# Kernel optimization log

Hardware: AMD Instinct MI355X
Metric: run time of the kernel (lower is better)

Reference implementation:

```python
import jax, jax.numpy as jnp
import numpy as np
import math

B, S, D = 2, 2048, 1024
H = 16
HD = D // H  # 64


def setup_inputs() -> dict:
    key = jax.random.key(0)
    ks = jax.random.split(key, 5)
    scale = 0.02
    x = jax.random.normal(ks[0], (B, S, D), dtype=jnp.float32)
    # torch Linear weights stored as [in, out] (already transposed)
    w_qkv = jax.random.normal(ks[1], (D, 3 * D), dtype=jnp.float32) * scale
    b_qkv = jnp.zeros((3 * D,), dtype=jnp.float32)
    w_proj = jax.random.normal(ks[2], (D, D), dtype=jnp.float32) * scale
    b_proj = jnp.zeros((D,), dtype=jnp.float32)
    return {"x": x, "w_qkv": w_qkv, "b_qkv": b_qkv, "w_proj": w_proj, "b_proj": b_proj}


def reference(x, w_qkv, b_qkv, w_proj, b_proj):
    b, s, d = x.shape
    qkv = x @ w_qkv + b_qkv                              # [B,S,3D]
    qkv = qkv.reshape(b, s, 3, H, HD)
    qkv = jnp.transpose(qkv, (2, 0, 3, 1, 4))            # [3,B,H,S,HD]
    q, k, v = qkv[0], qkv[1], qkv[2]
    present = jnp.concatenate([k, v], axis=0)            # [2B,H,S,HD]
    # scaled causal attention, full [B,H,S,S] scores as in the original
    attn = jnp.einsum('bhqd,bhkd->bhqk', q, k) * (1.0 / math.sqrt(HD))
    causal = jnp.tril(jnp.ones((s, s), dtype=bool))
    attn = jnp.where(causal[None, None], attn, -jnp.inf)
    attn = jax.nn.softmax(attn, axis=-1)
    out = jnp.einsum('bhqk,bhkd->bhqd', attn, v)         # [B,H,S,HD]
    out = jnp.transpose(out, (0, 2, 1, 3)).reshape(b, s, d)
    out = out @ w_proj + b_proj                          # NOTE: original module has project layer; see notes
    return (out, present)
```

## Files before the change

kernel.cpp:

```cpp
#include <hip/hip_runtime.h>
#include <hip/hip_bf16.h>

typedef short s16x8 __attribute__((ext_vector_type(8)));
typedef short s16x4 __attribute__((ext_vector_type(4)));
typedef float f32x4 __attribute__((ext_vector_type(4)));
typedef float f32x16 __attribute__((ext_vector_type(16)));
typedef unsigned int u32x4 __attribute__((ext_vector_type(4)));

#define S_LEN 2048
#define DMODEL 1024
#define NHEAD 16
#define HDIM 64
#define OUT_ELEMS 4194304
#define HEAD_ELEMS 4194304
#define SCALE_LOG2 0.1803368801111204f

__device__ inline short f2bf(float f) {
  __hip_bfloat16 h = __float2bfloat16(f);
  return __builtin_bit_cast(short, h);
}

__device__ inline f32x4 mfma16(s16x8 a, s16x8 b, f32x4 c) {
  return __builtin_amdgcn_mfma_f32_16x16x32_bf16(a, b, c, 0, 0, 0);
}
__device__ inline f32x16 mfma32(s16x8 a, s16x8 b, f32x16 c) {
  return __builtin_amdgcn_mfma_f32_32x32x16_bf16(a, b, c, 0, 0, 0);
}

__global__ __launch_bounds__(256) void transpose_cvt(
    const float* __restrict__ in, short* __restrict__ out, int R, int C) {
  int g = blockIdx.x * 256 + threadIdx.x;
  int c = g % C;
  int r0 = (g / C) * 8;
  s16x8 v;
#pragma unroll
  for (int j = 0; j < 8; j++) v[j] = f2bf(in[(size_t)(r0 + j) * C + c]);
  *(s16x8*)&out[(size_t)c * R + r0] = v;
}

template <int MODE, bool AF32>
__global__ __launch_bounds__(256) void gemm_bt(
    const void* __restrict__ Araw, const short* __restrict__ Bt,
    const float* __restrict__ bias, short* __restrict__ Ob0,
    float* __restrict__ Of, short* __restrict__ VtOut,
    short* __restrict__ KwOut, int M, int N, int K) {
  __shared__ short As[128][40];
  __shared__ short Bs[128][40];
  const int t = threadIdx.x;
  const int lane = t & 63;
  const int wid = t >> 6;
  const int wr = wid >> 1, wc = wid & 1;
  const int l16 = lane & 15, lg = lane >> 4;
  const int mbase = blockIdx.y * 128;
  const int nbase = blockIdx.x * 128;

  f32x4 acc[4][4];
#pragma unroll
  for (int m = 0; m < 4; m++)
#pragma unroll
    for (int n = 0; n < 4; n++) acc[m][n] = (f32x4){0.f, 0.f, 0.f, 0.f};

  const int srow = t >> 2;
  const int skc = (t & 3) * 8;

  for (int k0 = 0; k0 < K; k0 += 32) {
    s16x8 a0, a1;
    if constexpr (AF32) {
      const float* Af = (const float*)Araw;
      const float* p0 = &Af[(size_t)(mbase + srow) * K + k0 + skc];
      const float* p1 = &Af[(size_t)(mbase + srow + 64) * K + k0 + skc];
      f32x4 x00 = *(const f32x4*)p0, x01 = *(const f32x4*)(p0 + 4);
      f32x4 x10 = *(const f32x4*)p1, x11 = *(const f32x4*)(p1 + 4);
#pragma unroll
      for (int j = 0; j < 4; j++) {
        a0[j] = f2bf(x00[j]); a0[4 + j] = f2bf(x01[j]);
        a1[j] = f2bf(x10[j]); a1[4 + j] = f2bf(x11[j]);
      }
    } else {
      const short* Ab = (const short*)Araw;
      a0 = *(const s16x8*)&Ab[(size_t)(mbase + srow) * K + k0 + skc];
      a1 = *(const s16x8*)&Ab[(size_t)(mbase + srow + 64) * K + k0 + skc];
    }
    s16x8 b0 = *(const s16x8*)&Bt[(size_t)(nbase + srow) * K + k0 + skc];
    s16x8 b1 = *(const s16x8*)&Bt[(size_t)(nbase + srow + 64) * K + k0 + skc];
    __syncthreads();
    *(s16x8*)&As[srow][skc] = a0;
    *(s16x8*)&As[srow + 64][skc] = a1;
    *(s16x8*)&Bs[srow][skc] = b0;
    *(s16x8*)&Bs[srow + 64][skc] = b1;
    __syncthreads();
    s16x8 af[4], bfr[4];
#pragma unroll
    for (int m = 0; m < 4; m++)
      af[m] = *(const s16x8*)&As[wr * 64 + m * 16 + l16][lg * 8];
#pragma unroll
    for (int n = 0; n < 4; n++)
      bfr[n] = *(const s16x8*)&Bs[wc * 64 + n * 16 + l16][lg * 8];
#pragma unroll
    for (int m = 0; m < 4; m++)
#pragma unroll
      for (int n = 0; n < 4; n++)
        acc[m][n] = mfma16(af[m], bfr[n], acc[m][n]);
  }

#pragma unroll
  for (int m = 0; m < 4; m++) {
#pragma unroll
    for (int n = 0; n < 4; n++) {
      int gcol = nbase + wc * 64 + n * 16 + l16;
      float bv = bias[gcol];
      int part = gcol >> 10;
      int cin = gcol & 1023;
      int h = cin >> 6, hd = cin & 63;
      int grow0 = mbase + wr * 64 + m * 16 + lg * 4;
      float vr[4];
#pragma unroll
      for (int r = 0; r < 4; r++) vr[r] = acc[m][n][r] + bv;
      if (MODE == 0) {
        int bb = grow0 >> 11, s0 = grow0 & 2047;
        size_t base = ((size_t)(bb * NHEAD + h) * S_LEN + s0) * HDIM + hd;
        if (part == 0) {
#pragma unroll
          for (int r = 0; r < 4; r++)
            Ob0[base + (size_t)r * HDIM] = f2bf(vr[r] * SCALE_LOG2);
        } else if (part == 1) {
#pragma unroll
          for (int r = 0; r < 4; r++) Of[base + (size_t)r * HDIM] = vr[r];
          if (KwOut) {
#pragma unroll
            for (int r = 0; r < 4; r++)
              KwOut[base + (size_t)r * HDIM] = f2bf(vr[r]);
          }
        } else {
#pragma unroll
          for (int r = 0; r < 4; r++)
            Of[HEAD_ELEMS + base + (size_t)r * HDIM] = vr[r];
          s16x4 pk;
#pragma unroll
          for (int r = 0; r < 4; r++) pk[r] = f2bf(vr[r]);
          int w32 = s0 & 31;
          int nw = ((w32 >> 4) << 4) | ((w32 & 4) << 1) | ((w32 & 8) >> 1);
          int sperm = (s0 & ~31) | nw;
          *(s16x4*)&VtOut[((size_t)(bb * NHEAD + h) * HDIM + hd) * S_LEN +
                          sperm] = pk;
        }
      } else {
#pragma unroll
        for (int r = 0; r < 4; r++) Of[(size_t)(grow0 + r) * N + gcol] = vr[r];
      }
    }
  }
}

__global__ __launch_bounds__(256, 2) void attn_fwd_kbf16(
    const short* __restrict__ Q, const short* __restrict__ K,
    const short* __restrict__ Vt, short* __restrict__ AO) {
  __shared__ short Ks[2][64][64];
  __shared__ short Vs[2][64][64];

  const int p = blockIdx.x;
  const int bh = p & 31;
  const int seg = (p >> 5) & 7;
  const int qi = (p < 256) ? (15 - seg) : seg;
  const int qb = qi * 128;
  const int nt = 2 * qi + 2;

  const int tid = threadIdx.x;
  const int w = tid >> 6;
  const int lane = tid & 63;
  const int l32 = lane & 31;
  const int hi = lane >> 5;
  const int rsub = lane >> 3;
  const int sub = lane & 7;

  const short* Qb = Q + (size_t)bh * (S_LEN * HDIM);
  const short* Kb = K + (size_t)bh * (S_LEN * HDIM);
  const short* Vb = Vt + (size_t)bh * (HDIM * S_LEN);
  const int b = bh >> 4, h = bh & 15;

  const int qrow = qb + 32 * w + l32;
  const int qminw = qb + 32 * w;
  const int qmaxw = qminw + 31;

  s16x8 qf[4];
#pragma unroll
  for (int c = 0; c < 4; c++)
    qf[c] = *(const s16x8*)&Qb[(size_t)qrow * HDIM + c * 16 + hi * 8];

  f32x16 acc0 = {0.f}, acc1 = {0.f};
  float m = -1e30f, ll = 0.f;

  s16x8 kreg[2], vreg[2];
  auto LOADT = [&](int kt) {
    const int kb = kt * 64;
#pragma unroll
    for (int c = 0; c < 2; c++) {
      int row = 16 * w + 8 * c + rsub;
      int gs = sub ^ (row & 7);
      kreg[c] = *(const s16x8*)&Kb[(size_t)(kb + row) * HDIM + gs * 8];
      vreg[c] = *(const s16x8*)&Vb[(size_t)row * S_LEN + kb + gs * 8];
    }
  };
  auto WRITET = [&](int bb) {
#pragma unroll
    for (int c = 0; c < 2; c++) {
      int row = 16 * w + 8 * c + rsub;
      *(s16x8*)&Ks[bb][row][sub * 8] = kreg[c];
      *(s16x8*)&Vs[bb][row][sub * 8] = vreg[c];
    }
  };

  LOADT(0);
  WRITET(0);
  __syncthreads();
  int cur = 0;

#pragma unroll 1
  for (int kt = 0; kt < nt; kt++) {
    const int kb = kt * 64;
    if (kt + 1 < nt) LOADT(kt + 1);
    if (kb <= qmaxw) {
      f32x16 S0 = {0.f}, S1 = {0.f};
#pragma unroll
      for (int c = 0; c < 4; c++) {
        int cs = c * 2 + hi;
        int r0 = l32;
        int r1 = 32 + l32;
        s16x8 k0 = *(const s16x8*)&Ks[cur][r0][(cs ^ (r0 & 7)) * 8];
        s16x8 k1 = *(const s16x8*)&Ks[cur][r1][(cs ^ (r1 & 7)) * 8];
        S0 = mfma32(k0, qf[c], S0);
        S1 = mfma32(k1, qf[c], S1);
      }
      if (kb + 63 > qminw) {
#pragma unroll
        for (int r = 0; r < 16; r++) {
          int key0 = kb + (r & 3) + 8 * (r >> 2) + 4 * hi;
          S0[r] = (key0 <= qrow) ? S0[r] : -1e30f;
          S1[r] = (key0 + 32 <= qrow) ? S1[r] : -1e30f;
        }
      }
      float t8[8];
#pragma unroll
      for (int r = 0; r < 8; r++)
        t8[r] = fmaxf(fmaxf(S0[2 * r], S0[2 * r + 1]),
                      fmaxf(S1[2 * r], S1[2 * r + 1]));
      float tmax = fmaxf(fmaxf(fmaxf(t8[0], t8[1]), fmaxf(t8[2], t8[3])),
                         fmaxf(fmaxf(t8[4], t8[5]), fmaxf(t8[6], t8[7])));
      tmax = fmaxf(tmax, __shfl_xor(tmax, 32));
      if (!__all(tmax <= m + 11.0f)) {
        float mn = fmaxf(m, tmax);
        float alpha = __builtin_amdgcn_exp2f(m - mn);
        ll *= alpha;
#pragma unroll
        for (int r = 0; r < 16; r++) {
          acc0[r] *= alpha;
          acc1[r] *= alpha;
        }
        m = mn;
      }
#pragma unroll
      for (int r = 0; r < 16; r++) {
        S0[r] = __builtin_amdgcn_exp2f(S0[r] - m);
        S1[r] = __builtin_amdgcn_exp2f(S1[r] - m);
      }
      float s8[8];
#pragma unroll
      for (int r = 0; r < 8; r++)
        s8[r] = (S0[2 * r] + S0[2 * r + 1]) + (S1[2 * r] + S1[2 * r + 1]);
      float rs = ((s8[0] + s8[1]) + (s8[2] + s8[3])) +
                 ((s8[4] + s8[5]) + (s8[6] + s8[7]));
      rs += __shfl_xor(rs, 32);
      ll += rs;
#pragma unroll
      for (int half = 0; half < 2; half++) {
        const f32x16& S = half ? S1 : S0;
        u32x4 pbAv, pbBv;
#pragma unroll
        for (int g = 0; g < 4; g++) {
          unsigned int lo = (unsigned short)f2bf(S[2 * g]);
          unsigned int h16 = (unsigned short)f2bf(S[2 * g + 1]);
          pbAv[g] = lo | (h16 << 16);
          unsigned int lo2 = (unsigned short)f2bf(S[8 + 2 * g]);
          unsigned int h162 = (unsigned short)f2bf(S[9 + 2 * g]);
          pbBv[g] = lo2 | (h162 << 16);
        }
#pragma unroll
        for (int gg = 0; gg < 2; gg++) {
          s16x8 pb = __builtin_bit_cast(s16x8, gg ? pbBv : pbAv);
          int cs = (half * 2 + gg) * 2 + hi;
          int v0r = l32;
          int v1r = 32 + l32;
          s16x8 va0 = *(const s16x8*)&Vs[cur][v0r][(cs ^ (v0r & 7)) * 8];
          s16x8 va1 = *(const s16x8*)&Vs[cur][v1r][(cs ^ (v1r & 7)) * 8];
          acc0 = mfma32(va0, pb, acc0);
          acc1 = mfma32(va1, pb, acc1);
        }
      }
    }
    if (kt + 1 < nt) WRITET(cur ^ 1);
    __syncthreads();
    cur ^= 1;
  }

  float inv = 1.f / ll;
  size_t rowbase = ((size_t)(b * S_LEN + qrow)) * DMODEL + h * HDIM;
#pragma unroll
  for (int g = 0; g < 4; g++) {
    s16x4 o0, o1;
#pragma unroll
    for (int u = 0; u < 4; u++) {
      o0[u] = f2bf(acc0[4 * g + u] * inv);
      o1[u] = f2bf(acc1[4 * g + u] * inv);
    }
    *(s16x4*)&AO[rowbase + 8 * g + 4 * hi] = o0;
    *(s16x4*)&AO[rowbase + 32 + 8 * g + 4 * hi] = o1;
  }
}

__global__ __launch_bounds__(256, 4) void attn_fwd_kf32(
    const short* __restrict__ Q, const float* __restrict__ Kraw,
    const short* __restrict__ Vt, short* __restrict__ AO) {
  __shared__ float XFER[2][64][37];
  const int p = blockIdx.x;
  const int xcd = p & 7;
  const int rank = p >> 3;
  const int bh = (xcd << 2) | (rank >> 5);
  const int pr = rank & 31;
  const int tid = threadIdx.x;
  const int w = tid >> 6;
  const int lane = tid & 63;
  const int l32 = lane & 31;
  const int hi = lane >> 5;
  const short* Qb = Q + (size_t)bh * (S_LEN * HDIM);
  const short* Vb = Vt + (size_t)bh * (HDIM * S_LEN);
  const float* Kb32 = Kraw + (size_t)bh * (S_LEN * HDIM);
  const int b = bh >> 4, h = bh & 15;

#pragma unroll 1
  for (int ph = 0; ph < 2; ph++) {
    const int j = ph ? pr : 63 - pr;
    const int qb = j * 32;
    s16x8 qf[4];
#pragma unroll
    for (int c = 0; c < 4; c++)
      qf[c] = *(const s16x8*)&Qb[(size_t)(qb + l32) * HDIM + c * 16 + hi * 8];
    f32x16 acc0 = {0.f}, acc1 = {0.f};
    float m = -1e30f, ll = 0.f;
#pragma unroll 1
    for (int kt = w; kt <= j; kt += 4) {
      const int kb = kt * 32;
      f32x16 S = {0.f};
#pragma unroll
      for (int c = 0; c < 4; c++) {
        const float* kr = &Kb32[(size_t)(kb + l32) * HDIM + c * 16 + hi * 8];
        f32x4 k0 = *(const f32x4*)kr, k1 = *(const f32x4*)(kr + 4);
        s16x8 kf;
#pragma unroll
        for (int u = 0; u < 4; u++) {
          kf[u] = f2bf(k0[u]);
          kf[4 + u] = f2bf(k1[u]);
        }
        S = mfma32(kf, qf[c], S);
      }
      const short* vr0 = &Vb[(size_t)l32 * S_LEN + kb + hi * 8];
      const short* vr1 = &Vb[(size_t)(32 + l32) * S_LEN + kb + hi * 8];
      s16x8 va00 = *(const s16x8*)vr0;
      s16x8 va01 = *(const s16x8*)(vr0 + 16);
      s16x8 va10 = *(const s16x8*)vr1;
      s16x8 va11 = *(const s16x8*)(vr1 + 16);
      if (kt == j) {
#pragma unroll
        for (int r = 0; r < 16; r++) {
          int keyl = (r & 3) + 8 * (r >> 2) + 4 * hi;
          S[r] = (keyl <= l32) ? S[r] : -1e30f;
        }
      }
      float t8[8];
#pragma unroll
      for (int r = 0; r < 8; r++) t8[r] = fmaxf(S[2 * r], S[2 * r + 1]);
      float tmax = fmaxf(fmaxf(fmaxf(t8[0], t8[1]), fmaxf(t8[2], t8[3])),
                         fmaxf(fmaxf(t8[4], t8[5]), fmaxf(t8[6], t8[7])));
      tmax = fmaxf(tmax, __shfl_xor(tmax, 32));
      if (!__all(tmax <= m + 11.0f)) {
        float mn = fmaxf(m, tmax);
        float alpha = __builtin_amdgcn_exp2f(m - mn);
        ll *= alpha;
#pragma unroll
        for (int r = 0; r < 16; r++) {
          acc0[r] *= alpha;
          acc1[r] *= alpha;
        }
        m = mn;
      }
#pragma unroll
      for (int r = 0; r < 16; r++) S[r] = __builtin_amdgcn_exp2f(S[r] - m);
      float s8[8];
#pragma unroll
      for (int r = 0; r < 8; r++) s8[r] = S[2 * r] + S[2 * r + 1];
      float rs = ((s8[0] + s8[1]) + (s8[2] + s8[3])) +
                 ((s8[4] + s8[5]) + (s8[6] + s8[7]));
      rs += __shfl_xor(rs, 32);
      ll += rs;
      u32x4 pb0v, pb1v;
#pragma unroll
      for (int g = 0; g < 4; g++) {
        unsigned int lo = (unsigned short)f2bf(S[2 * g]);
        unsigned int h16 = (unsigned short)f2bf(S[2 * g + 1]);
        pb0v[g] = lo | (h16 << 16);
        unsigned int lo2 = (unsigned short)f2bf(S[8 + 2 * g]);
        unsigned int h162 = (unsigned short)f2bf(S[9 + 2 * g]);
        pb1v[g] = lo2 | (h162 << 16);
      }
      s16x8 pb0 = __builtin_bit_cast(s16x8, pb0v);
      s16x8 pb1 = __builtin_bit_cast(s16x8, pb1v);
      acc0 = mfma32(va00, pb0, acc0);
      acc1 = mfma32(va10, pb0, acc1);
      acc0 = mfma32(va01, pb1, acc0);
      acc1 = mfma32(va11, pb1, acc1);
    }
    if (w & 1) {
      float* dst = &XFER[w >> 1][lane][0];
      dst[0] = m; dst[1] = ll;
#pragma unroll
      for (int r = 0; r < 16; r++) { dst[2 + r] = acc0[r]; dst[18 + r] = acc1[r]; }
    }
    __syncthreads();
    if (!(w & 1)) {
      const float* src = &XFER[w >> 1][lane][0];
      float m2 = src[0], l2 = src[1];
      float M = fmaxf(m, m2);
      float a1 = __builtin_amdgcn_exp2f(m - M);
      float a2 = __builtin_amdgcn_exp2f(m2 - M);
      ll = ll * a1 + l2 * a2;
#pragma unroll
      for (int r = 0; r < 16; r++) {
        acc0[r] = acc0[r] * a1 + src[2 + r] * a2;
        acc1[r] = acc1[r] * a1 + src[18 + r] * a2;
      }
      m = M;
    }
    __syncthreads();
    if (w == 2) {
      float* dst = &XFER[0][lane][0];
      dst[0] = m; dst[1] = ll;
#pragma unroll
      for (int r = 0; r < 16; r++) { dst[2 + r] = acc0[r]; dst[18 + r] = acc1[r]; }
    }
    __syncthreads();
    if (w == 0) {
      const float* src = &XFER[0][lane][0];
      float m2 = src[0], l2 = src[1];
      float M = fmaxf(m, m2);
      float a1 = __builtin_amdgcn_exp2f(m - M);
      float a2 = __builtin_amdgcn_exp2f(m2 - M);
      ll = ll * a1 + l2 * a2;
#pragma unroll
      for (int r = 0; r < 16; r++) {
        acc0[r] = acc0[r] * a1 + src[2 + r] * a2;
        acc1[r] = acc1[r] * a1 + src[18 + r] * a2;
      }
      float inv = 1.f / ll;
      size_t rowbase = ((size_t)(b * S_LEN + qb + l32)) * DMODEL + h * HDIM;
#pragma unroll
      for (int g = 0; g < 4; g++) {
        s16x4 o0, o1;
#pragma unroll
        for (int u = 0; u < 4; u++) {
          o0[u] = f2bf(acc0[4 * g + u] * inv);
          o1[u] = f2bf(acc1[4 * g + u] * inv);
        }
        *(s16x4*)&AO[rowbase + 8 * g + 4 * hi] = o0;
        *(s16x4*)&AO[rowbase + 32 + 8 * g + 4 * hi] = o1;
      }
    }
    __syncthreads();
  }
}

extern "C" void kernel_launch(void* const* d_in, const int* in_sizes, int n_in,
                              void* d_out, int out_size, void* d_ws,
                              size_t ws_size, hipStream_t stream) {
  const float* x = (const float*)d_in[0];
  const float* w_qkv = (const float*)d_in[1];
  const float* b_qkv = (const float*)d_in[2];
  const float* w_proj = (const float*)d_in[3];
  const float* b_proj = (const float*)d_in[4];
  float* out = (float*)d_out;
  float* presentK = out + OUT_ELEMS;

  short* ws = (short*)d_ws;
  const bool kbf16 = ws_size >= (size_t)35651584;

  short *Qw, *Vt, *wprojT, *wqkvT, *attnout, *Kw;
  if (kbf16) {
    Qw = ws;
    Kw = ws + 4194304;
    Vt = ws + 8388608;
    wprojT = ws + 12582912;
    wqkvT = ws + 13631488;
    attnout = ws + 13631488;
  } else {
    if (ws_size < (size_t)27262976) return;
    Qw = ws;
    Vt = ws + 4194304;
    wprojT = ws + 8388608;
    wqkvT = ws + 9437184;
    attnout = ws + 9437184;
    Kw = nullptr;
  }

  transpose_cvt<<<dim3(1536), 256, 0, stream>>>(w_qkv, wqkvT, 1024, 3072);
  transpose_cvt<<<dim3(512), 256, 0, stream>>>(w_proj, wprojT, 1024, 1024);
  gemm_bt<0, true><<<dim3(24, 32), 256, 0, stream>>>(
      x, wqkvT, b_qkv, Qw, presentK, Vt, Kw, 4096, 3072, 1024);
  if (kbf16)
    attn_fwd_kbf16<<<dim3(512), 256, 0, stream>>>(Qw, Kw, Vt, attnout);
  else
    attn_fwd_kf32<<<dim3(1024), 256, 0, stream>>>(Qw, presentK, Vt, attnout);
  gemm_bt<1, false><<<dim3(8, 32), 256, 0, stream>>>(
      attnout, wprojT, b_proj, nullptr, out, nullptr, nullptr, 4096, 1024,
      1024);
}
```

Before: 131.0 us.

## Pre-convert x to bf16 and stage GEMM tiles via direct global-to-LDS loads

Adds a separate kernel that converts x to bf16 into the output buffer as scratch, so the QKV GEMM reads only bf16 operands. Both GEMMs now use the global_load_lds builtin to copy 16-byte chunks straight into shared memory, bypassing registers. The padding is removed from the LDS tiles, which raises the risk of bank conflicts on fragment reads. It also adds an extra launch and an extra pass over x.

```diff
diff --git a/kernel.cpp b/kernel.cpp
--- a/kernel.cpp
+++ b/kernel.cpp
@@ -27,6 +27,27 @@
   return __builtin_amdgcn_mfma_f32_32x32x16_bf16(a, b, c, 0, 0, 0);
 }
 
+typedef __attribute__((address_space(1))) const void gvoid;
+typedef __attribute__((address_space(3))) void lvoid;
+__device__ inline void gload_lds16(const void* g, void* l) {
+  __builtin_amdgcn_global_load_lds((gvoid*)g, (lvoid*)l, 16, 0, 0);
+}
+
+__global__ __launch_bounds__(256) void cvt_bf16(const float* __restrict__ in,
+                                                short* __restrict__ out) {
+  int g = blockIdx.x * 256 + threadIdx.x;
+  const float* p = &in[(size_t)g * 8];
+  f32x4 a = *(const f32x4*)p;
+  f32x4 b = *(const f32x4*)(p + 4);
+  s16x8 v;
+#pragma unroll
+  for (int j = 0; j < 4; j++) {
+    v[j] = f2bf(a[j]);
+    v[4 + j] = f2bf(b[j]);
+  }
+  *(s16x8*)&out[(size_t)g * 8] = v;
+}
+
 __global__ __launch_bounds__(256) void transpose_cvt(
     const float* __restrict__ in, short* __restrict__ out, int R, int C) {
   int g = blockIdx.x * 256 + threadIdx.x;
@@ -38,14 +59,14 @@
   *(s16x8*)&out[(size_t)c * R + r0] = v;
 }
 
-template <int MODE, bool AF32>
+template <int MODE>
 __global__ __launch_bounds__(256) void gemm_bt(
-    const void* __restrict__ Araw, const short* __restrict__ Bt,
+    const short* __restrict__ A, const short* __restrict__ Bt,
     const float* __restrict__ bias, short* __restrict__ Ob0,
     float* __restrict__ Of, short* __restrict__ VtOut,
     short* __restrict__ KwOut, int M, int N, int K) {
-  __shared__ short As[128][40];
-  __shared__ short Bs[128][40];
+  __shared__ short As[128 * 32];
+  __shared__ short Bs[128 * 32];
   const int t = threadIdx.x;
   const int lane = t & 63;
   const int wid = t >> 6;
@@ -60,42 +81,29 @@
 #pragma unroll
     for (int n = 0; n < 4; n++) acc[m][n] = (f32x4){0.f, 0.f, 0.f, 0.f};
 
-  const int srow = t >> 2;
-  const int skc = (t & 3) * 8;
+  const int srow = lane >> 2;
+  const int scol = (lane & 3) * 8;
+  const short* Ag = &A[(size_t)(mbase + wid * 32 + srow) * K + scol];
+  const short* Bg = &Bt[(size_t)(nbase + wid * 32 + srow) * K + scol];
+  short* AsW0 = &As[(wid * 32) * 32];
+  short* AsW1 = &As[(wid * 32 + 16) * 32];
+  short* BsW0 = &Bs[(wid * 32) * 32];
+  short* BsW1 = &Bs[(wid * 32 + 16) * 32];
 
   for (int k0 = 0; k0 < K; k0 += 32) {
-    s16x8 a0, a1;
-    if constexpr (AF32) {
-      const float* Af = (const float*)Araw;
-      const float* p0 = &Af[(size_t)(mbase + srow) * K + k0 + skc];
-      const float* p1 = &Af[(size_t)(mbase + srow + 64) * K + k0 + skc];
-      f32x4 x00 = *(const f32x4*)p0, x01 = *(const f32x4*)(p0 + 4);
-      f32x4 x10 = *(const f32x4*)p1, x11 = *(const f32x4*)(p1 + 4);
-#pragma unroll
-      for (int j = 0; j < 4; j++) {
-        a0[j] = f2bf(x00[j]); a0[4 + j] = f2bf(x01[j]);
-        a1[j] = f2bf(x10[j]); a1[4 + j] = f2bf(x11[j]);
-      }
-    } else {
-      const short* Ab = (const short*)Araw;
-      a0 = *(const s16x8*)&Ab[(size_t)(mbase + srow) * K + k0 + skc];
-      a1 = *(const s16x8*)&Ab[(size_t)(mbase + srow + 64) * K + k0 + skc];
-    }
-    s16x8 b0 = *(const s16x8*)&Bt[(size_t)(nbase + srow) * K + k0 + skc];
-    s16x8 b1 = *(const s16x8*)&Bt[(size_t)(nbase + srow + 64) * K + k0 + skc];
-    __syncthreads();
-    *(s16x8*)&As[srow][skc] = a0;
-    *(s16x8*)&As[srow + 64][skc] = a1;
-    *(s16x8*)&Bs[srow][skc] = b0;
-    *(s16x8*)&Bs[srow + 64][skc] = b1;
+    __syncthreads();
+    gload_lds16(Ag + k0, AsW0);
+    gload_lds16(Ag + (size_t)16 * K + k0, AsW1);
+    gload_lds16(Bg + k0, BsW0);
+    gload_lds16(Bg + (size_t)16 * K + k0, BsW1);
     __syncthreads();
     s16x8 af[4], bfr[4];
 #pragma unroll
     for (int m = 0; m < 4; m++)
-      af[m] = *(const s16x8*)&As[wr * 64 + m * 16 + l16][lg * 8];
+      af[m] = *(const s16x8*)&As[(wr * 64 + m * 16 + l16) * 32 + lg * 8];
 #pragma unroll
     for (int n = 0; n < 4; n++)
-      bfr[n] = *(const s16x8*)&Bs[wc * 64 + n * 16 + l16][lg * 8];
+      bfr[n] = *(const s16x8*)&Bs[(wc * 64 + n * 16 + l16) * 32 + lg * 8];
 #pragma unroll
     for (int m = 0; m < 4; m++)
 #pragma unroll
@@ -488,6 +496,8 @@
   float* out = (float*)d_out;
   float* presentK = out + OUT_ELEMS;
 
+  short* xbf = (short*)out;
+
   short* ws = (short*)d_ws;
   const bool kbf16 = ws_size >= (size_t)35651584;
 
@@ -509,15 +519,16 @@
     Kw = nullptr;
   }
 
+  cvt_bf16<<<dim3(2048), 256, 0, stream>>>(x, xbf);
   transpose_cvt<<<dim3(1536), 256, 0, stream>>>(w_qkv, wqkvT, 1024, 3072);
   transpose_cvt<<<dim3(512), 256, 0, stream>>>(w_proj, wprojT, 1024, 1024);
-  gemm_bt<0, true><<<dim3(24, 32), 256, 0, stream>>>(
-      x, wqkvT, b_qkv, Qw, presentK, Vt, Kw, 4096, 3072, 1024);
+  gemm_bt<0><<<dim3(24, 32), 256, 0, stream>>>(
+      xbf, wqkvT, b_qkv, Qw, presentK, Vt, Kw, 4096, 3072, 1024);
   if (kbf16)
     attn_fwd_kbf16<<<dim3(512), 256, 0, stream>>>(Qw, Kw, Vt, attnout);
   else
     attn_fwd_kf32<<<dim3(1024), 256, 0, stream>>>(Qw, presentK, Vt, attnout);
-  gemm_bt<1, false><<<dim3(8, 32), 256, 0, stream>>>(
+  gemm_bt<1><<<dim3(8, 32), 256, 0, stream>>>(
       attnout, wprojT, b_proj, nullptr, out, nullptr, nullptr, 4096, 1024,
       1024);
 }
```

Result: no change. 131.1 us (+0.1%).
